# Optimization experiments

Measured on AMD Instinct MI355X. Metric: run time of the kernel, lower is better.

Reference implementation:

```python
import jax, jax.numpy as jnp
from jax import lax
import numpy as np

NUM_LAYERS = 6
KERNEL = 3
FILTERS = 64
STENCIL = 4
IN_CH = 3  # C, vx, vy
SHIFT = 0.0
VAR = 1.0


def periodic_conv(x, w, b):
    # x: [B,H,W,Cin], w: [k,k,Cin,Cout] -> periodic ('wrap') padding + VALID conv
    p = w.shape[0] // 2
    xp = jnp.pad(x, ((0, 0), (p, p), (p, p), (0, 0)), mode='wrap')
    y = lax.conv_general_dilated(xp, w, (1, 1), 'VALID',
                                 dimension_numbers=('NHWC', 'HWIO', 'NHWC'))
    return y + b


def stencil_shift_tensors(c, size):
    # c: [B,H,W] -> [B,H,W,size*size] of periodically rolled copies
    half = size // 2
    shifts = [jnp.roll(c, shift=(half - i, half - j), axis=(1, 2))
              for i in range(size) for j in range(size)]
    return jnp.stack(shifts, axis=-1)


def setup_inputs() -> dict:
    key = jax.random.key(0)
    ks = jax.random.split(key, 16)
    B, H, W = 8, 256, 256
    inp = {
        'C': jax.random.normal(ks[0], (B, H, W), jnp.float32),
        'vx': jax.random.normal(ks[1], (B, H, W), jnp.float32),
        'vy': jax.random.normal(ks[2], (B, H, W), jnp.float32),
    }
    fan_in0 = KERNEL * KERNEL * IN_CH
    inp['w0'] = jax.random.normal(ks[3], (KERNEL, KERNEL, IN_CH, FILTERS), jnp.float32) / np.sqrt(fan_in0)
    inp['b0'] = jnp.zeros((FILTERS,), jnp.float32)
    fan_in = KERNEL * KERNEL * FILTERS
    for i in range(1, NUM_LAYERS - 1):
        inp[f'w{i}'] = jax.random.normal(ks[3 + i], (KERNEL, KERNEL, FILTERS, FILTERS), jnp.float32) / np.sqrt(fan_in)
        inp[f'b{i}'] = jnp.zeros((FILTERS,), jnp.float32)
    inp['wout'] = jax.random.normal(ks[10], (KERNEL, KERNEL, FILTERS, STENCIL * STENCIL), jnp.float32) / np.sqrt(fan_in)
    inp['bout'] = jnp.zeros((STENCIL * STENCIL,), jnp.float32)
    return inp


def reference(C, vx, vy, w0, b0, w1, b1, w2, b2, w3, b3, w4, b4, wout, bout):
    ws = [w0, w1, w2, w3, w4]
    bs = [b0, b1, b2, b3, b4]
    x = jnp.stack([(C - SHIFT) / VAR, vx, vy], axis=-1)  # [B,H,W,3]
    for w, b in zip(ws, bs):
        x = jax.nn.relu(periodic_conv(x, w, b))
    coeffs = periodic_conv(x, wout, bout)  # [B,H,W,S^2]
    stencil = stencil_shift_tensors(C, STENCIL)  # [B,H,W,S^2]
    # einsum 'ijkl,ijkl->ijk'
    return jnp.einsum('bhws,bhws->bhw', coeffs, stencil)
```

## Files before the change

### kernel.cpp

```cpp
#include <hip/hip_runtime.h>
#include <hip/hip_bf16.h>


#define HW   256
#define MASK 255
#define CH   64
#define TX   32
#define TY   16

typedef short bf16x8 __attribute__((ext_vector_type(8)));
typedef float f32x4  __attribute__((ext_vector_type(4)));

__device__ __forceinline__ float bf2f(unsigned short u) {
    return __uint_as_float(((unsigned int)u) << 16);
}
__device__ __forceinline__ unsigned short f2bf(float f) {
    unsigned int x = __float_as_uint(f);
    return (unsigned short)((x + 0x7fffu + ((x >> 16) & 1u)) >> 16);
}

__global__ __launch_bounds__(512) void k_layer0(
    const float* __restrict__ Cin, const float* __restrict__ vx,
    const float* __restrict__ vy, const float* __restrict__ w0,
    const float* __restrict__ b0, unsigned short* __restrict__ out)
{
    int t  = threadIdx.x;
    int lx = t & 31, ly = t >> 5;
    int x  = blockIdx.x * TX + lx;
    int y  = blockIdx.y * TY + ly;
    int bb = blockIdx.z;
    int pbase = bb * HW * HW;

    float a[27];
#pragma unroll
    for (int ky = 0; ky < 3; ky++) {
        int yy = (y + ky - 1) & MASK;
#pragma unroll
        for (int kx = 0; kx < 3; kx++) {
            int xx  = (x + kx - 1) & MASK;
            int idx = pbase + yy * HW + xx;
            a[(ky * 3 + kx) * 3 + 0] = Cin[idx];
            a[(ky * 3 + kx) * 3 + 1] = vx[idx];
            a[(ky * 3 + kx) * 3 + 2] = vy[idx];
        }
    }

    size_t obase = ((size_t)(pbase + y * HW + x)) * CH;
    for (int c4 = 0; c4 < 4; c4++) {
        float acc[16];
#pragma unroll
        for (int j = 0; j < 16; j++) acc[j] = b0[c4 * 16 + j];
#pragma unroll
        for (int k = 0; k < 27; k++) {
            float av = a[k];
            const float* wq = w0 + k * CH + c4 * 16;
#pragma unroll
            for (int j = 0; j < 16; j++) acc[j] = fmaf(av, wq[j], acc[j]);
        }
        unsigned short o[16];
#pragma unroll
        for (int j = 0; j < 16; j++) o[j] = f2bf(fmaxf(acc[j], 0.f));
        *reinterpret_cast<uint4*>(out + obase + c4 * 16)     = *reinterpret_cast<uint4*>(o);
        *reinterpret_cast<uint4*>(out + obase + c4 * 16 + 8) = *reinterpret_cast<uint4*>(o + 8);
    }
}

#define MT 32

__global__ __launch_bounds__(512, 2) void k_mid_mfma(
    const unsigned short* __restrict__ in, const float* __restrict__ w,
    const float* __restrict__ b, unsigned short* __restrict__ out)
{
    __shared__ unsigned short sAct[34 * 34 * CH];
    __shared__ unsigned short sWb[4096];

    const int t    = threadIdx.x;
    const int lane = t & 63;
    const int wid  = t >> 6;
    const int l15  = lane & 15;
    const int l4   = lane >> 4;
    const int x0   = blockIdx.x * MT;
    const int y0   = blockIdx.y * MT;
    const size_t pbase = (size_t)blockIdx.z * HW * HW;

    for (int g = t; g < 34 * 34 * 8; g += 512) {
        int hp = g >> 3, cg = g & 7;
        int hr = hp / 34, hc = hp - hr * 34;
        int gy = (y0 + hr - 1) & MASK;
        int gx = (x0 + hc - 1) & MASK;
        uint4 v = *reinterpret_cast<const uint4*>(
            in + ((pbase + gy * HW + gx) * CH + cg * 8));
        *reinterpret_cast<uint4*>(&sAct[hp * 64 + ((cg ^ (hp & 7)) << 3)]) = v;
    }

    const int wco  = t & 63;
    const int wq   = t >> 6;
    const int wci0 = (wq >> 2) * 32 + (wq & 3) * 8;
    float wr[8];
#pragma unroll
    for (int j = 0; j < 8; j++)
        wr[j] = w[(0 * 64 + wci0 + j) * 64 + wco];

    __syncthreads();

    {
        unsigned short o8[8];
#pragma unroll
        for (int j = 0; j < 8; j++) o8[j] = f2bf(wr[j]);
        *reinterpret_cast<uint4*>(&sWb[t * 8]) = *reinterpret_cast<uint4*>(o8);
#pragma unroll
        for (int j = 0; j < 8; j++)
            wr[j] = w[(1 * 64 + wci0 + j) * 64 + wco];
    }
    __syncthreads();

    f32x4 acc[8][4];
#pragma unroll
    for (int m = 0; m < 8; m++)
#pragma unroll
        for (int n = 0; n < 4; n++) {
            float bv = b[n * 16 + l15];
            acc[m][n] = (f32x4){bv, bv, bv, bv};
        }

    int pxb[8];
#pragma unroll
    for (int m = 0; m < 8; m++)
        pxb[m] = (4 * wid + (m >> 1)) * 34 + (m & 1) * 16 + l15;

    const int wbbase = (l4 << 9) + (l15 << 3);

    for (int tap = 0; tap < 9; tap++) {
        const int koff = (tap / 3) * 34 + (tap % 3);

#pragma unroll
        for (int s = 0; s < 2; s++) {
            bf16x8 bf[4];
#pragma unroll
            for (int n = 0; n < 4; n++)
                bf[n] = *reinterpret_cast<const bf16x8*>(
                    &sWb[wbbase + (s << 11) + (n << 7)]);
            bf16x8 af[8];
            const int o = s * 4 + l4;
#pragma unroll
            for (int m = 0; m < 8; m++) {
                int px  = pxb[m] + koff;
                int off = (px << 6) + (((o ^ px) & 7) << 3);
                af[m] = *reinterpret_cast<const bf16x8*>(&sAct[off]);
            }
#pragma unroll
            for (int m = 0; m < 8; m++)
#pragma unroll
                for (int n = 0; n < 4; n++)
                    acc[m][n] = __builtin_amdgcn_mfma_f32_16x16x32_bf16(
                        af[m], bf[n], acc[m][n], 0, 0, 0);
        }

        __syncthreads();
        if (tap < 8) {
            unsigned short o8[8];
#pragma unroll
            for (int j = 0; j < 8; j++) o8[j] = f2bf(wr[j]);
            *reinterpret_cast<uint4*>(&sWb[t * 8]) = *reinterpret_cast<uint4*>(o8);
            if (tap < 7) {
#pragma unroll
                for (int j = 0; j < 8; j++)
                    wr[j] = w[((tap + 2) * 64 + wci0 + j) * 64 + wco];
            }
            __syncthreads();
        }
    }

#pragma unroll
    for (int m = 0; m < 8; m++) {
        int y = y0 + 4 * wid + (m >> 1);
        int x = x0 + (m & 1) * 16;
        unsigned short* pm = out + (pbase + y * HW + x) * CH + (l4 << 8) + l15;
#pragma unroll
        for (int n = 0; n < 4; n++)
#pragma unroll
            for (int j = 0; j < 4; j++)
                pm[j * 64 + n * 16] = f2bf(fmaxf(acc[m][n][j], 0.f));
    }
}

__global__ __launch_bounds__(512, 2) void k_out_mfma(
    const unsigned short* __restrict__ in, const float* __restrict__ w,
    const float* __restrict__ b, const float* __restrict__ Cin,
    float* __restrict__ out)
{
    __shared__ unsigned short sAct[18 * 34 * CH];
    __shared__ unsigned short sW[9 * 128 * 8];
    __shared__ float sC[19 * 35];

    const int t    = threadIdx.x;
    const int lane = t & 63;
    const int wid  = t >> 6;
    const int l15  = lane & 15;
    const int l4   = lane >> 4;
    const int x0   = blockIdx.x * 32;
    const int y0   = blockIdx.y * 16;
    const size_t pbase = (size_t)blockIdx.z * HW * HW;

    for (int g = t; g < 18 * 34 * 8; g += 512) {
        int hp = g >> 3, cg = g & 7;
        int hr = hp / 34, hc = hp - hr * 34;
        int gy = (y0 + hr - 1) & MASK;
        int gx = (x0 + hc - 1) & MASK;
        uint4 v = *reinterpret_cast<const uint4*>(
            in + ((pbase + gy * HW + gx) * CH + cg * 8));
        *reinterpret_cast<uint4*>(&sAct[hp * 64 + ((cg ^ (hp & 7)) << 3)]) = v;
    }
    for (int g = t; g < 1152; g += 512) {
        int tap = g >> 7, s = (g >> 6) & 1, dl = g & 63;
        int ci0 = s * 32 + (dl >> 4) * 8;
        int co  = dl & 15;
        unsigned short o8[8];
#pragma unroll
        for (int j = 0; j < 8; j++)
            o8[j] = f2bf(w[(tap * 64 + ci0 + j) * 16 + co]);
        *reinterpret_cast<uint4*>(&sW[g * 8]) = *reinterpret_cast<uint4*>(o8);
    }
    for (int g = t; g < 19 * 35; g += 512) {
        int r = g / 35, c2 = g - r * 35;
        int gy = (y0 + r - 2) & MASK;
        int gx = (x0 + c2 - 2) & MASK;
        sC[g] = Cin[pbase + gy * HW + gx];
    }
    __syncthreads();

    f32x4 acc[4];
    {
        float bv = b[l15];
#pragma unroll
        for (int m = 0; m < 4; m++) acc[m] = (f32x4){bv, bv, bv, bv};
    }

    int pxb[4];
#pragma unroll
    for (int m = 0; m < 4; m++)
        pxb[m] = (2 * wid + (m >> 1)) * 34 + (m & 1) * 16 + l15;

    for (int tap = 0; tap < 9; tap++) {
        const int koff = (tap / 3) * 34 + (tap % 3);
#pragma unroll
        for (int s = 0; s < 2; s++) {
            bf16x8 bf = *reinterpret_cast<const bf16x8*>(
                &sW[((tap * 2 + s) << 9) + (lane << 3)]);
            const int o = s * 4 + l4;
#pragma unroll
            for (int m = 0; m < 4; m++) {
                int px  = pxb[m] + koff;
                int off = (px << 6) + (((o ^ px) & 7) << 3);
                bf16x8 af = *reinterpret_cast<const bf16x8*>(&sAct[off]);
                acc[m] = __builtin_amdgcn_mfma_f32_16x16x32_bf16(
                    af, bf, acc[m], 0, 0, 0);
            }
        }
    }

#pragma unroll
    for (int m = 0; m < 4; m++) {
        int py = 2 * wid + (m >> 1);
        int xb = (m & 1) * 16 + l4 * 4;
#pragma unroll
        for (int j = 0; j < 4; j++) {
            int xt = xb + j;
            float v = acc[m][j] * sC[(py + (l15 >> 2)) * 35 + xt + (l15 & 3)];
            v += __shfl_xor(v, 1);
            v += __shfl_xor(v, 2);
            v += __shfl_xor(v, 4);
            v += __shfl_xor(v, 8);
            if (l15 == 0)
                out[pbase + (y0 + py) * HW + x0 + xt] = v;
        }
    }
}

extern "C" void kernel_launch(void* const* d_in, const int* in_sizes, int n_in,
                              void* d_out, int out_size, void* d_ws, size_t ws_size,
                              hipStream_t stream)
{
    (void)in_sizes; (void)n_in; (void)out_size; (void)ws_size;
    const float* Cin  = (const float*)d_in[0];
    const float* vx   = (const float*)d_in[1];
    const float* vy   = (const float*)d_in[2];
    const float* w0   = (const float*)d_in[3];
    const float* b0   = (const float*)d_in[4];
    const float* w1   = (const float*)d_in[5];
    const float* b1   = (const float*)d_in[6];
    const float* w2   = (const float*)d_in[7];
    const float* b2   = (const float*)d_in[8];
    const float* w3   = (const float*)d_in[9];
    const float* b3   = (const float*)d_in[10];
    const float* w4   = (const float*)d_in[11];
    const float* b4   = (const float*)d_in[12];
    const float* wout = (const float*)d_in[13];
    const float* bout = (const float*)d_in[14];

    unsigned short* actA = (unsigned short*)d_ws;
    unsigned short* actB = actA + (size_t)8 * HW * HW * CH;

    dim3 block(512);
    dim3 grid0(HW / TX, HW / TY, 8);
    dim3 gridM(HW / MT, HW / MT, 8);
    dim3 gridO(HW / 32, HW / 16, 8);

    k_layer0  <<<grid0, block, 0, stream>>>(Cin, vx, vy, w0, b0, actA);
    k_mid_mfma<<<gridM, block, 0, stream>>>(actA, w1, b1, actB);
    k_mid_mfma<<<gridM, block, 0, stream>>>(actB, w2, b2, actA);
    k_mid_mfma<<<gridM, block, 0, stream>>>(actA, w3, b3, actB);
    k_mid_mfma<<<gridM, block, 0, stream>>>(actB, w4, b4, actA);
    k_out_mfma<<<gridO, block, 0, stream>>>(actA, wout, bout, Cin, (float*)d_out);
}
```

Baseline: 285.3 us.

## Rewrite mid conv layers to read activations from global/L2 with 32x32 MFMA

```diff
diff --git a/kernel.cpp b/kernel.cpp
--- a/kernel.cpp
+++ b/kernel.cpp
@@ -10,6 +10,7 @@
 
 typedef short bf16x8 __attribute__((ext_vector_type(8)));
 typedef float f32x4  __attribute__((ext_vector_type(4)));
+typedef float f32x16 __attribute__((ext_vector_type(16)));
 
 __device__ __forceinline__ float bf2f(unsigned short u) {
     return __uint_as_float(((unsigned int)u) << 16);
@@ -65,122 +66,91 @@
     }
 }
 
-#define MT 32
-
-__global__ __launch_bounds__(512, 2) void k_mid_mfma(
+__global__ __launch_bounds__(512, 2) void k_mid_l2(
     const unsigned short* __restrict__ in, const float* __restrict__ w,
     const float* __restrict__ b, unsigned short* __restrict__ out)
 {
-    __shared__ unsigned short sAct[34 * 34 * CH];
-    __shared__ unsigned short sWb[4096];
+    __shared__ unsigned short sW[4608 * 8];
 
     const int t    = threadIdx.x;
     const int lane = t & 63;
-    const int wid  = t >> 6;
-    const int l15  = lane & 15;
-    const int l4   = lane >> 4;
-    const int x0   = blockIdx.x * MT;
-    const int y0   = blockIdx.y * MT;
-    const size_t pbase = (size_t)blockIdx.z * HW * HW;
-
-    for (int g = t; g < 34 * 34 * 8; g += 512) {
-        int hp = g >> 3, cg = g & 7;
-        int hr = hp / 34, hc = hp - hr * 34;
-        int gy = (y0 + hr - 1) & MASK;
-        int gx = (x0 + hc - 1) & MASK;
-        uint4 v = *reinterpret_cast<const uint4*>(
-            in + ((pbase + gy * HW + gx) * CH + cg * 8));
-        *reinterpret_cast<uint4*>(&sAct[hp * 64 + ((cg ^ (hp & 7)) << 3)]) = v;
-    }
-
-    const int wco  = t & 63;
-    const int wq   = t >> 6;
-    const int wci0 = (wq >> 2) * 32 + (wq & 3) * 8;
-    float wr[8];
-#pragma unroll
-    for (int j = 0; j < 8; j++)
-        wr[j] = w[(0 * 64 + wci0 + j) * 64 + wco];
-
+    const int wv   = t >> 6;
+    const int l31  = lane & 31;
+    const int l5   = lane >> 5;
+
+    const int bid = blockIdx.x;
+    const int tid = (bid & 7) * 128 + (bid >> 3);
+    const int bz  = tid >> 7;
+    const int rr  = tid & 127;
+    const int y0  = (rr >> 3) * 16;
+    const int x0  = (rr & 7) * 32;
+    const size_t pbase = (size_t)bz * HW * HW;
+
+    for (int g = t; g < 4608; g += 512) {
+        int gl = g & 63, gn = (g >> 6) & 1, gk = (g >> 7) & 3, gtap = g >> 9;
+        const float* wp = w + (gtap * 64 + gk * 16 + ((gl >> 5) << 3)) * 64
+                            + gn * 32 + (gl & 31);
+        unsigned short o8[8];
+#pragma unroll
+        for (int j = 0; j < 8; j++) o8[j] = f2bf(wp[j * 64]);
+        *reinterpret_cast<uint4*>(&sW[g * 8]) = *reinterpret_cast<uint4*>(o8);
+    }
     __syncthreads();
 
+    f32x16 acc[2][2];
     {
-        unsigned short o8[8];
-#pragma unroll
-        for (int j = 0; j < 8; j++) o8[j] = f2bf(wr[j]);
-        *reinterpret_cast<uint4*>(&sWb[t * 8]) = *reinterpret_cast<uint4*>(o8);
-#pragma unroll
-        for (int j = 0; j < 8; j++)
-            wr[j] = w[(1 * 64 + wci0 + j) * 64 + wco];
-    }
-    __syncthreads();
-
-    f32x4 acc[8][4];
-#pragma unroll
-    for (int m = 0; m < 8; m++)
-#pragma unroll
-        for (int n = 0; n < 4; n++) {
-            float bv = b[n * 16 + l15];
-            acc[m][n] = (f32x4){bv, bv, bv, bv};
-        }
-
-    int pxb[8];
-#pragma unroll
-    for (int m = 0; m < 8; m++)
-        pxb[m] = (4 * wid + (m >> 1)) * 34 + (m & 1) * 16 + l15;
-
-    const int wbbase = (l4 << 9) + (l15 << 3);
-
+        float bv0 = b[l31], bv1 = b[32 + l31];
+#pragma unroll
+        for (int m = 0; m < 2; m++)
+#pragma unroll
+            for (int j = 0; j < 16; j++) {
+                acc[m][0][j] = bv0;
+                acc[m][1][j] = bv1;
+            }
+    }
+
+    int xoff[3];
+#pragma unroll
+    for (int kx = 0; kx < 3; kx++)
+        xoff[kx] = ((x0 + l31 + kx - 1) & MASK) * CH + l5 * 8;
+
+    const unsigned short* inb = in + pbase * CH;
+
+#pragma unroll
     for (int tap = 0; tap < 9; tap++) {
-        const int koff = (tap / 3) * 34 + (tap % 3);
-
-#pragma unroll
-        for (int s = 0; s < 2; s++) {
-            bf16x8 bf[4];
-#pragma unroll
-            for (int n = 0; n < 4; n++)
-                bf[n] = *reinterpret_cast<const bf16x8*>(
-                    &sWb[wbbase + (s << 11) + (n << 7)]);
-            bf16x8 af[8];
-            const int o = s * 4 + l4;
-#pragma unroll
-            for (int m = 0; m < 8; m++) {
-                int px  = pxb[m] + koff;
-                int off = (px << 6) + (((o ^ px) & 7) << 3);
-                af[m] = *reinterpret_cast<const bf16x8*>(&sAct[off]);
-            }
-#pragma unroll
-            for (int m = 0; m < 8; m++)
-#pragma unroll
-                for (int n = 0; n < 4; n++)
-                    acc[m][n] = __builtin_amdgcn_mfma_f32_16x16x32_bf16(
-                        af[m], bf[n], acc[m][n], 0, 0, 0);
-        }
-
-        __syncthreads();
-        if (tap < 8) {
-            unsigned short o8[8];
-#pragma unroll
-            for (int j = 0; j < 8; j++) o8[j] = f2bf(wr[j]);
-            *reinterpret_cast<uint4*>(&sWb[t * 8]) = *reinterpret_cast<uint4*>(o8);
-            if (tap < 7) {
-#pragma unroll
-                for (int j = 0; j < 8; j++)
-                    wr[j] = w[((tap + 2) * 64 + wci0 + j) * 64 + wco];
-            }
-            __syncthreads();
-        }
-    }
-
-#pragma unroll
-    for (int m = 0; m < 8; m++) {
-        int y = y0 + 4 * wid + (m >> 1);
-        int x = x0 + (m & 1) * 16;
-        unsigned short* pm = out + (pbase + y * HW + x) * CH + (l4 << 8) + l15;
-#pragma unroll
-        for (int n = 0; n < 4; n++)
-#pragma unroll
-            for (int j = 0; j < 4; j++)
-                pm[j * 64 + n * 16] = f2bf(fmaxf(acc[m][n][j], 0.f));
+        const int ky = tap / 3, kx = tap % 3;
+        const unsigned short* r0 =
+            inb + (size_t)((y0 + 2 * wv + 0 + ky - 1) & MASK) * (HW * CH);
+        const unsigned short* r1 =
+            inb + (size_t)((y0 + 2 * wv + 1 + ky - 1) & MASK) * (HW * CH);
+#pragma unroll
+        for (int k = 0; k < 4; k++) {
+            bf16x8 a0 = *reinterpret_cast<const bf16x8*>(r0 + xoff[kx] + k * 16);
+            bf16x8 a1 = *reinterpret_cast<const bf16x8*>(r1 + xoff[kx] + k * 16);
+            bf16x8 b0 = *reinterpret_cast<const bf16x8*>(
+                &sW[(((tap * 4 + k) * 2 + 0) * 64 + lane) * 8]);
+            bf16x8 b1 = *reinterpret_cast<const bf16x8*>(
+                &sW[(((tap * 4 + k) * 2 + 1) * 64 + lane) * 8]);
+            acc[0][0] = __builtin_amdgcn_mfma_f32_32x32x16_bf16(a0, b0, acc[0][0], 0, 0, 0);
+            acc[0][1] = __builtin_amdgcn_mfma_f32_32x32x16_bf16(a0, b1, acc[0][1], 0, 0, 0);
+            acc[1][0] = __builtin_amdgcn_mfma_f32_32x32x16_bf16(a1, b0, acc[1][0], 0, 0, 0);
+            acc[1][1] = __builtin_amdgcn_mfma_f32_32x32x16_bf16(a1, b1, acc[1][1], 0, 0, 0);
+        }
+    }
+
+#pragma unroll
+    for (int m = 0; m < 2; m++) {
+        const int y = y0 + 2 * wv + m;
+        unsigned short* ob = out + (pbase + (size_t)y * HW + x0) * CH + l31;
+#pragma unroll
+        for (int n = 0; n < 2; n++)
+#pragma unroll
+            for (int r4 = 0; r4 < 4; r4++)
+#pragma unroll
+                for (int j = 0; j < 4; j++) {
+                    int r = j + 8 * r4 + 4 * l5;
+                    ob[r * CH + n * 32] = f2bf(fmaxf(acc[m][n][r4 * 4 + j], 0.f));
+                }
     }
 }
 
@@ -303,13 +273,13 @@
 
     dim3 block(512);
     dim3 grid0(HW / TX, HW / TY, 8);
-    dim3 gridM(HW / MT, HW / MT, 8);
+    dim3 gridM(1024);
     dim3 gridO(HW / 32, HW / 16, 8);
 
     k_layer0  <<<grid0, block, 0, stream>>>(Cin, vx, vy, w0, b0, actA);
-    k_mid_mfma<<<gridM, block, 0, stream>>>(actA, w1, b1, actB);
-    k_mid_mfma<<<gridM, block, 0, stream>>>(actB, w2, b2, actA);
-    k_mid_mfma<<<gridM, block, 0, stream>>>(actA, w3, b3, actB);
-    k_mid_mfma<<<gridM, block, 0, stream>>>(actB, w4, b4, actA);
+    k_mid_l2  <<<gridM, block, 0, stream>>>(actA, w1, b1, actB);
+    k_mid_l2  <<<gridM, block, 0, stream>>>(actB, w2, b2, actA);
+    k_mid_l2  <<<gridM, block, 0, stream>>>(actA, w3, b3, actB);
+    k_mid_l2  <<<gridM, block, 0, stream>>>(actB, w4, b4, actA);
     k_out_mfma<<<gridO, block, 0, stream>>>(actA, wout, bout, Cin, (float*)d_out);
 }
```

Measured after the change: 386.5 us. 1.35x slower.

## Prepack mid-layer weights to bf16 fragments and swizzle blocks across XCDs

Applied to the files above, without the earlier changes.

```diff
diff --git a/kernel.cpp b/kernel.cpp
--- a/kernel.cpp
+++ b/kernel.cpp
@@ -17,6 +17,26 @@
 __device__ __forceinline__ unsigned short f2bf(float f) {
     unsigned int x = __float_as_uint(f);
     return (unsigned short)((x + 0x7fffu + ((x >> 16) & 1u)) >> 16);
+}
+
+__global__ __launch_bounds__(512) void k_pack(
+    const float* __restrict__ w1, const float* __restrict__ w2,
+    const float* __restrict__ w3, const float* __restrict__ w4,
+    unsigned short* __restrict__ dst)
+{
+    int g = blockIdx.x * 512 + threadIdx.x;
+    if (g >= 4 * 4608) return;
+    int L = g / 4608, r = g - L * 4608;
+    const float* w = (L == 0) ? w1 : (L == 1) ? w2 : (L == 2) ? w3 : w4;
+    int q = r >> 8, n = (r >> 6) & 3, l = r & 63;
+    int tap = q >> 1, s = q & 1;
+    int ci0 = s * 32 + ((l >> 4) << 3);
+    int co  = n * 16 + (l & 15);
+    unsigned short o8[8];
+#pragma unroll
+    for (int j = 0; j < 8; j++)
+        o8[j] = f2bf(w[(tap * 64 + ci0 + j) * 64 + co]);
+    *reinterpret_cast<uint4*>(dst + (size_t)g * 8) = *reinterpret_cast<uint4*>(o8);
 }
 
 __global__ __launch_bounds__(512) void k_layer0(
@@ -67,21 +87,26 @@
 
 #define MT 32
 
-__global__ __launch_bounds__(512, 2) void k_mid_mfma(
-    const unsigned short* __restrict__ in, const float* __restrict__ w,
+__global__ __launch_bounds__(512, 2) void k_mid_v4(
+    const unsigned short* __restrict__ in,
+    const unsigned short* __restrict__ wp,
     const float* __restrict__ b, unsigned short* __restrict__ out)
 {
     __shared__ unsigned short sAct[34 * 34 * CH];
-    __shared__ unsigned short sWb[4096];
 
     const int t    = threadIdx.x;
     const int lane = t & 63;
     const int wid  = t >> 6;
     const int l15  = lane & 15;
     const int l4   = lane >> 4;
-    const int x0   = blockIdx.x * MT;
-    const int y0   = blockIdx.y * MT;
-    const size_t pbase = (size_t)blockIdx.z * HW * HW;
+
+    const int bid = blockIdx.x;
+    const int tid = (bid & 7) * 64 + (bid >> 3);
+    const int bz  = tid >> 6;
+    const int rr  = tid & 63;
+    const int y0  = (rr >> 3) * MT;
+    const int x0  = (rr & 7) * MT;
+    const size_t pbase = (size_t)bz * HW * HW;
 
     for (int g = t; g < 34 * 34 * 8; g += 512) {
         int hp = g >> 3, cg = g & 7;
@@ -93,25 +118,11 @@
         *reinterpret_cast<uint4*>(&sAct[hp * 64 + ((cg ^ (hp & 7)) << 3)]) = v;
     }
 
-    const int wco  = t & 63;
-    const int wq   = t >> 6;
-    const int wci0 = (wq >> 2) * 32 + (wq & 3) * 8;
-    float wr[8];
-#pragma unroll
-    for (int j = 0; j < 8; j++)
-        wr[j] = w[(0 * 64 + wci0 + j) * 64 + wco];
-
-    __syncthreads();
-
-    {
-        unsigned short o8[8];
-#pragma unroll
-        for (int j = 0; j < 8; j++) o8[j] = f2bf(wr[j]);
-        *reinterpret_cast<uint4*>(&sWb[t * 8]) = *reinterpret_cast<uint4*>(o8);
-#pragma unroll
-        for (int j = 0; j < 8; j++)
-            wr[j] = w[(1 * 64 + wci0 + j) * 64 + wco];
-    }
+    bf16x8 bnx[4];
+#pragma unroll
+    for (int n = 0; n < 4; n++)
+        bnx[n] = *reinterpret_cast<const bf16x8*>(wp + (size_t)(n * 512 + lane * 8));
+
     __syncthreads();
 
     f32x4 acc[8][4];
@@ -128,46 +139,32 @@
     for (int m = 0; m < 8; m++)
         pxb[m] = (4 * wid + (m >> 1)) * 34 + (m & 1) * 16 + l15;
 
-    const int wbbase = (l4 << 9) + (l15 << 3);
-
+#pragma unroll
     for (int tap = 0; tap < 9; tap++) {
         const int koff = (tap / 3) * 34 + (tap % 3);
-
 #pragma unroll
         for (int s = 0; s < 2; s++) {
-            bf16x8 bf[4];
-#pragma unroll
-            for (int n = 0; n < 4; n++)
-                bf[n] = *reinterpret_cast<const bf16x8*>(
-                    &sWb[wbbase + (s << 11) + (n << 7)]);
-            bf16x8 af[8];
+            const int q = tap * 2 + s;
+            bf16x8 bc[4];
+#pragma unroll
+            for (int n = 0; n < 4; n++) bc[n] = bnx[n];
+            if (q < 17) {
+#pragma unroll
+                for (int n = 0; n < 4; n++)
+                    bnx[n] = *reinterpret_cast<const bf16x8*>(
+                        wp + (size_t)(((q + 1) * 4 + n) * 512 + lane * 8));
+            }
             const int o = s * 4 + l4;
 #pragma unroll
             for (int m = 0; m < 8; m++) {
                 int px  = pxb[m] + koff;
                 int off = (px << 6) + (((o ^ px) & 7) << 3);
-                af[m] = *reinterpret_cast<const bf16x8*>(&sAct[off]);
-            }
-#pragma unroll
-            for (int m = 0; m < 8; m++)
+                bf16x8 af = *reinterpret_cast<const bf16x8*>(&sAct[off]);
 #pragma unroll
                 for (int n = 0; n < 4; n++)
                     acc[m][n] = __builtin_amdgcn_mfma_f32_16x16x32_bf16(
-                        af[m], bf[n], acc[m][n], 0, 0, 0);
-        }
-
-        __syncthreads();
-        if (tap < 8) {
-            unsigned short o8[8];
-#pragma unroll
-            for (int j = 0; j < 8; j++) o8[j] = f2bf(wr[j]);
-            *reinterpret_cast<uint4*>(&sWb[t * 8]) = *reinterpret_cast<uint4*>(o8);
-            if (tap < 7) {
-#pragma unroll
-                for (int j = 0; j < 8; j++)
-                    wr[j] = w[((tap + 2) * 64 + wci0 + j) * 64 + wco];
+                        af, bc[n], acc[m][n], 0, 0, 0);
             }
-            __syncthreads();
         }
     }
 
@@ -175,7 +172,7 @@
     for (int m = 0; m < 8; m++) {
         int y = y0 + 4 * wid + (m >> 1);
         int x = x0 + (m & 1) * 16;
-        unsigned short* pm = out + (pbase + y * HW + x) * CH + (l4 << 8) + l15;
+        unsigned short* pm = out + (pbase + (size_t)y * HW + x) * CH + (l4 << 8) + l15;
 #pragma unroll
         for (int n = 0; n < 4; n++)
 #pragma unroll
@@ -301,15 +298,18 @@
     unsigned short* actA = (unsigned short*)d_ws;
     unsigned short* actB = actA + (size_t)8 * HW * HW * CH;
 
+    unsigned short* wpk = (unsigned short*)d_out;
+
     dim3 block(512);
     dim3 grid0(HW / TX, HW / TY, 8);
-    dim3 gridM(HW / MT, HW / MT, 8);
+    dim3 gridM(512);
     dim3 gridO(HW / 32, HW / 16, 8);
 
+    k_pack    <<<36, block, 0, stream>>>(w1, w2, w3, w4, wpk);
     k_layer0  <<<grid0, block, 0, stream>>>(Cin, vx, vy, w0, b0, actA);
-    k_mid_mfma<<<gridM, block, 0, stream>>>(actA, w1, b1, actB);
-    k_mid_mfma<<<gridM, block, 0, stream>>>(actB, w2, b2, actA);
-    k_mid_mfma<<<gridM, block, 0, stream>>>(actA, w3, b3, actB);
-    k_mid_mfma<<<gridM, block, 0, stream>>>(actB, w4, b4, actA);
+    k_mid_v4  <<<gridM, block, 0, stream>>>(actA, wpk + 0 * 36864, b1, actB);
+    k_mid_v4  <<<gridM, block, 0, stream>>>(actB, wpk + 1 * 36864, b2, actA);
+    k_mid_v4  <<<gridM, block, 0, stream>>>(actA, wpk + 2 * 36864, b3, actB);
+    k_mid_v4  <<<gridM, block, 0, stream>>>(actB, wpk + 3 * 36864, b4, actA);
     k_out_mfma<<<gridO, block, 0, stream>>>(actA, wout, bout, Cin, (float*)d_out);
 }
```

New measurement: 265.0 us. -7.1%, faster.
